# Kernel optimization log

Hardware: AMD Instinct MI355X
Metric: run time of the kernel (lower is better)

Reference implementation:

```python
import jax, jax.numpy as jnp
import numpy as np

HEADS = 8

def _conv1d(x, w, b, pad, groups):
    # x: (B, C_in, T), w: (C_out, C_in/groups, K)
    out = jax.lax.conv_general_dilated(
        x, w, window_strides=(1,), padding=[(pad, pad)],
        feature_group_count=groups,
        dimension_numbers=('NCH', 'OIH', 'NCH'))
    if b is not None:
        out = out + b[None, :, None]
    return out


def setup_inputs() -> dict:
    key = jax.random.key(0)
    ks = jax.random.split(key, 9)
    B, T, D, H = 8, 4096, 512, HEADS
    s = 0.02
    return {
        'x': jax.random.normal(ks[0], (B, T, D), jnp.float32),
        'W_qkv': jax.random.normal(ks[1], (D, 3 * D), jnp.float32) * s,
        'w_qkv_dw': jax.random.normal(ks[2], (3 * D, 1, 3), jnp.float32) * s,
        'w_ctx1': jax.random.normal(ks[3], (D, 1, 3), jnp.float32) * s,
        'w_ctx2': jax.random.normal(ks[4], (D, 1, 5), jnp.float32) * s,
        'W_fc': jax.random.normal(ks[5], (3 * H, 9), jnp.float32) * s,
        'b_fc': jnp.zeros((9,), jnp.float32),
        'w_dep': jax.random.normal(ks[6], (D, 9, 3), jnp.float32) * s,
        'b_dep': jnp.zeros((D,), jnp.float32),
        'temperature': jnp.ones((H, 1, 1), jnp.float32),
    }


def reference(x, W_qkv, w_qkv_dw, w_ctx1, w_ctx2, W_fc, b_fc, w_dep, b_dep, temperature):
    B, T, D = x.shape
    H = HEADS
    C = D // H  # channels per head

    # qkv linear + depthwise conv (k=3)
    qkv = x @ W_qkv                                       # (B,T,3D)
    qkv = _conv1d(qkv.transpose(0, 2, 1), w_qkv_dw, None, 1, 3 * D).transpose(0, 2, 1)

    # fc branch: (B,T,3H,C) -> fc over the 3H axis -> (B,T,9,C)
    f_all = qkv.reshape(B, T, 3 * H, C)
    f = jnp.einsum('bthc,hn->btnc', f_all, W_fc) + b_fc[None, None, :, None]
    f_conv = f.reshape(B, T, 9 * C).transpose(0, 2, 1)    # (B, 9C, T)
    out_conv = _conv1d(f_conv, w_dep, b_dep, 1, C).transpose(0, 2, 1)  # (B,T,D)

    # channel attention: q,k,v -> (B,H,C,T), L2-normalize over T
    q, k, v = jnp.split(qkv, 3, axis=-1)
    def to_heads(z):
        return z.reshape(B, T, H, C).transpose(0, 2, 3, 1)  # (B,H,C,T)
    q, k, v = to_heads(q), to_heads(k), to_heads(v)
    q = q / jnp.maximum(jnp.linalg.norm(q, axis=-1, keepdims=True), 1e-12)
    k = k / jnp.maximum(jnp.linalg.norm(k, axis=-1, keepdims=True), 1e-12)
    attn = jnp.einsum('bhct,bhdt->bhcd', q, k) * temperature  # (B,H,C,C)
    attn = jax.nn.softmax(attn, axis=-1)
    out_att = jnp.einsum('bhcd,bhdt->bhct', attn, v)
    out_att = out_att.transpose(0, 3, 1, 2).reshape(B, T, D)

    # regional context: depthwise k=3 -> ReLU -> depthwise k=5
    ctx = _conv1d(x.transpose(0, 2, 1), w_ctx1, None, 1, D)
    ctx = jax.nn.relu(ctx)
    ctx = _conv1d(ctx, w_ctx2, None, 2, D).transpose(0, 2, 1)

    return ctx + out_conv + out_att
```

## Files before the change

kernel.cpp:

```cpp
#include <hip/hip_runtime.h>

typedef __attribute__((ext_vector_type(8))) _Float16 f16x8;
typedef __attribute__((ext_vector_type(4))) _Float16 f16x4;
typedef __attribute__((ext_vector_type(4))) float f32x4;

__device__ inline void gl_lds16(const void* g, void* l) {
  __builtin_amdgcn_global_load_lds(
      (const __attribute__((address_space(1))) unsigned int*)g,
      (__attribute__((address_space(3))) unsigned int*)l, 16, 0, 0);
}

__global__ __launch_bounds__(256) void zero_k(float* __restrict__ g, float* __restrict__ n) {
  int i = (blockIdx.x << 8) + threadIdx.x;
  if (i < 262144) g[i] = 0.f;
  if (i < 12288) n[i] = 0.f;
}

__global__ __launch_bounds__(256) void split_x_k(
    const float* __restrict__ x, _Float16* __restrict__ hi) {
  int i = (blockIdx.x << 8) + threadIdx.x;
  float4 v = ((const float4*)x)[i];
  f16x4 h;
  h[0] = (_Float16)v.x; h[1] = (_Float16)v.y;
  h[2] = (_Float16)v.z; h[3] = (_Float16)v.w;
  *(f16x4*)&hi[(size_t)i << 2] = h;
}

__global__ __launch_bounds__(256) void split_wt_k(
    const float* __restrict__ w, _Float16* __restrict__ hi) {
  __shared__ float tile[32][33];
  int k0 = blockIdx.x << 5;
  int n0 = blockIdx.y << 5;
  int r = threadIdx.x >> 5, c = threadIdx.x & 31;
#pragma unroll
  for (int i = 0; i < 4; ++i)
    tile[r + (i << 3)][c] = w[(size_t)(k0 + r + (i << 3)) * 1536 + n0 + c];
  __syncthreads();
#pragma unroll
  for (int i = 0; i < 4; ++i) {
    int n = r + (i << 3), k = c;
    hi[(size_t)(n0 + n) * 512 + k0 + k] = (_Float16)tile[k][n];
  }
}

__global__ __launch_bounds__(256) void gemm_qkv_k(
    const _Float16* __restrict__ xhi, const _Float16* __restrict__ whi,
    _Float16* __restrict__ qkv) {
  __shared__ _Float16 As[3][128 * 32];
  __shared__ _Float16 Bs[3][128 * 32];
  const int tid = threadIdx.x;
  const int wave = tid >> 6, lane = tid & 63;
  const int orig = blockIdx.x;
  const int wg = ((orig & 7) * 384) + (orig >> 3);
  const int bm = wg / 12;
  const int bn = wg - bm * 12;
  const int wm = (wave >> 1) << 6, wn = (wave & 1) << 6;
  const int lhi = lane >> 4, llo = lane & 15;

  f32x4 zero = {};
  f32x4 acc[4][4];
#pragma unroll
  for (int i = 0; i < 4; ++i)
#pragma unroll
    for (int j = 0; j < 4; ++j) acc[i][j] = zero;

  const int srowA = (bm << 7) + (wave << 5) + (lane >> 2);
  const int srowB = (bn << 7) + (wave << 5) + (lane >> 2);
  const int kc = (((lane & 3) ^ ((lane >> 3) & 3)) << 3);
  const size_t aoff0 = ((size_t)srowA << 9) + kc;
  const size_t aoff1 = ((size_t)(srowA + 16) << 9) + kc;
  const size_t boff0 = ((size_t)srowB << 9) + kc;
  const size_t boff1 = ((size_t)(srowB + 16) << 9) + kc;
  const int wb0 = (wave << 5) << 5;
  const int wb1 = ((wave << 5) + 16) << 5;

  auto stage = [&](int buf, int kk) {
    const int k0 = kk << 5;
    gl_lds16(xhi + aoff0 + k0, &As[buf][wb0]);
    gl_lds16(xhi + aoff1 + k0, &As[buf][wb1]);
    gl_lds16(whi + boff0 + k0, &Bs[buf][wb0]);
    gl_lds16(whi + boff1 + k0, &Bs[buf][wb1]);
  };

  stage(0, 0);
  stage(1, 1);
  int cur = 0;
  for (int kk = 0; kk < 16; ++kk) {
    if (kk < 14) {
      stage((cur + 2) % 3, kk + 2);
      asm volatile("s_waitcnt vmcnt(8)" ::: "memory");
    } else if (kk == 14) {
      asm volatile("s_waitcnt vmcnt(4)" ::: "memory");
    } else {
      asm volatile("s_waitcnt vmcnt(0)" ::: "memory");
    }
    __builtin_amdgcn_s_barrier();
    __builtin_amdgcn_sched_barrier(0);
    const int ksw = ((lhi ^ ((llo >> 1) & 3)) << 3);
    f16x8 af[4], bf[4];
#pragma unroll
    for (int mi = 0; mi < 4; ++mi)
      af[mi] = *(const f16x8*)&As[cur][((wm + (mi << 4) + llo) << 5) + ksw];
#pragma unroll
    for (int ni = 0; ni < 4; ++ni)
      bf[ni] = *(const f16x8*)&Bs[cur][((wn + (ni << 4) + llo) << 5) + ksw];
    __builtin_amdgcn_s_setprio(1);
#pragma unroll
    for (int mi = 0; mi < 4; ++mi)
#pragma unroll
      for (int ni = 0; ni < 4; ++ni)
        acc[mi][ni] = __builtin_amdgcn_mfma_f32_16x16x32_f16(af[mi], bf[ni], acc[mi][ni], 0, 0, 0);
    __builtin_amdgcn_s_setprio(0);
    __builtin_amdgcn_sched_barrier(0);
    __builtin_amdgcn_s_barrier();
    cur = (cur + 1) % 3;
  }
#pragma unroll
  for (int mi = 0; mi < 4; ++mi) {
    const int row0 = (bm << 7) + wm + (mi << 4) + (lhi << 2);
#pragma unroll
    for (int ni = 0; ni < 4; ++ni) {
      const int col = (bn << 7) + wn + (ni << 4) + llo;
      _Float16* p = qkv + (size_t)row0 * 1536 + col;
#pragma unroll
      for (int r = 0; r < 4; ++r) p[(size_t)r * 1536] = (_Float16)acc[mi][ni][r];
    }
  }
}

__global__ __launch_bounds__(384) void dwconv_k(
    const _Float16* __restrict__ qkv, const float* __restrict__ w3,
    _Float16* __restrict__ qkvc, float* __restrict__ partials) {
  __shared__ float ssb[192][8];
  const int tid = threadIdx.x;
  const int sub = (tid >= 192) ? 1 : 0;
  const int g = tid - sub * 192;
  const int c0 = g << 3;
  const int blk = blockIdx.x;
  const int b = blk >> 6;
  const int pair = blk & 63;
  const int t0 = (pair << 6) + (sub << 5);
  const _Float16* base = qkv + ((size_t)((b << 12) + t0)) * 1536 + c0;
  _Float16* obase = qkvc + ((size_t)((b << 12) + t0)) * 1536 + c0;
  float w0[8], w1[8], w2[8];
#pragma unroll
  for (int j = 0; j < 8; ++j) {
    w0[j] = w3[(c0 + j) * 3 + 0];
    w1[j] = w3[(c0 + j) * 3 + 1];
    w2[j] = w3[(c0 + j) * 3 + 2];
  }
  f16x8 zero8 = {};
  f16x8 pv = (t0 == 0) ? zero8 : *(const f16x8*)&base[-1536];
  f16x8 cv = *(const f16x8*)&base[0];
  float ss[8] = {};
#pragma unroll 4
  for (int i = 0; i < 32; ++i) {
    f16x8 nv = (t0 + i == 4095) ? zero8 : *(const f16x8*)&base[(size_t)(i + 1) * 1536];
    f16x8 o;
#pragma unroll
    for (int j = 0; j < 8; ++j) {
      float of = (float)pv[j] * w0[j] + (float)cv[j] * w1[j] + (float)nv[j] * w2[j];
      _Float16 oh = (_Float16)of;
      o[j] = oh;
      float orf = (float)oh;
      ss[j] += orf * orf;
    }
    *(f16x8*)&obase[(size_t)i * 1536] = o;
    pv = cv; cv = nv;
  }
  if (sub) {
#pragma unroll
    for (int j = 0; j < 8; ++j) ssb[g][j] = ss[j];
  }
  __syncthreads();
  if (!sub) {
    float* pp = partials + ((size_t)pair) * 12288 + b * 1536 + c0;
    *(float4*)pp = make_float4(ss[0] + ssb[g][0], ss[1] + ssb[g][1],
                               ss[2] + ssb[g][2], ss[3] + ssb[g][3]);
    *(float4*)(pp + 4) = make_float4(ss[4] + ssb[g][4], ss[5] + ssb[g][5],
                                     ss[6] + ssb[g][6], ss[7] + ssb[g][7]);
  }
}

__global__ __launch_bounds__(256) void reduce_norms_k(
    const float* __restrict__ partials, float* __restrict__ norms) {
  int i = (blockIdx.x << 8) + threadIdx.x;
  float s = 0.f;
  for (int ch = 0; ch < 64; ++ch) s += partials[(size_t)ch * 12288 + i];
  norms[i] = s;
}

__global__ __launch_bounds__(256) void attn_gram_k(
    const _Float16* __restrict__ qkvc, float* __restrict__ Gbuf) {
  int bh = blockIdx.x;  int b = bh >> 3, h = bh & 7;
  int tq = blockIdx.y;
  __shared__ _Float16 qT[64][136];
  __shared__ _Float16 kT[64][136];
  const int tid = threadIdx.x;
  const int wave = tid >> 6, lane = tid & 63;
  const int lhi = lane >> 4, llo = lane & 15;
  const int coff = h << 6;
  const int c0 = wave << 4;

  f32x4 zero = {};
  f32x4 acc[4];
#pragma unroll
  for (int i = 0; i < 4; ++i) acc[i] = zero;

  for (int ch = 0; ch < 2; ++ch) {
    __syncthreads();
#pragma unroll
    for (int i = 0; i < 4; ++i) {
      int idx = (i << 8) + tid;
      int tl = idx >> 3, g = idx & 7;
      int t = (tq << 8) + (ch << 7) + tl;
      const _Float16* gp = qkvc + ((size_t)((b << 12) + t)) * 1536 + coff + (g << 3);
      f16x8 qv = *(const f16x8*)gp;
      f16x8 kv = *(const f16x8*)(gp + 512);
#pragma unroll
      for (int j = 0; j < 8; ++j) {
        qT[(g << 3) + j][tl] = qv[j];
        kT[(g << 3) + j][tl] = kv[j];
      }
    }
    __syncthreads();
#pragma unroll
    for (int kt = 0; kt < 4; ++kt) {
      const int toff = (kt << 5) + (lhi << 3);
      f16x8 af = *(const f16x8*)&qT[c0 + llo][toff];
#pragma unroll
      for (int di = 0; di < 4; ++di) {
        f16x8 bf = *(const f16x8*)&kT[(di << 4) + llo][toff];
        acc[di] = __builtin_amdgcn_mfma_f32_16x16x32_f16(af, bf, acc[di], 0, 0, 0);
      }
    }
  }
  float* Gp = Gbuf + ((size_t)bh << 12);
#pragma unroll
  for (int di = 0; di < 4; ++di)
#pragma unroll
    for (int r = 0; r < 4; ++r)
      atomicAdd(&Gp[(c0 + (lhi << 2) + r) * 64 + (di << 4) + llo], acc[di][r]);
}

__global__ __launch_bounds__(256) void attn_softmax_k(
    const float* __restrict__ Gbuf, const float* __restrict__ norms,
    const float* __restrict__ temp, float* __restrict__ attn) {
  int tid = threadIdx.x;
  int sub = tid >> 6, c = tid & 63;
  int bh = (blockIdx.x << 2) + sub;
  int b = bh >> 3, h = bh & 7;
  __shared__ float nk[4][64];
  float nq = fmaxf(sqrtf(norms[b * 1536 + (h << 6) + c]), 1e-12f);
  nk[sub][c] = fmaxf(sqrtf(norms[b * 1536 + 512 + (h << 6) + c]), 1e-12f);
  __syncthreads();
  float inq = temp[h] / nq;
  const float* Gp = Gbuf + ((size_t)bh << 12) + c * 64;
  float mx = -3.0e38f;
  for (int d = 0; d < 64; ++d) mx = fmaxf(mx, Gp[d] / nk[sub][d] * inq);
  float s = 0.f;
  for (int d = 0; d < 64; ++d) s += expf(Gp[d] / nk[sub][d] * inq - mx);
  float inv = 1.0f / s;
  float* op = attn + ((size_t)bh << 12) + c * 64;
  for (int d = 0; d < 64; ++d) op[d] = expf(Gp[d] / nk[sub][d] * inq - mx) * inv;
}

__global__ __launch_bounds__(256) void attn_out_k(
    const _Float16* __restrict__ qkvc, const float* __restrict__ attn,
    float* __restrict__ out) {
  int blk = blockIdx.x;
  int tt = blk & 31, h = (blk >> 5) & 7, b = blk >> 8;
  int t0 = tt << 7;
  __shared__ float atT[64][68];
  __shared__ float vbT[64][132];
  int tid = threadIdx.x;
  const float* ap = attn + ((size_t)((b << 3) + h) << 12);
#pragma unroll
  for (int i = 0; i < 16; ++i) {
    int idx = (i << 8) + tid;  int c2 = idx >> 6, e = idx & 63;
    atT[e][c2] = ap[idx];
  }
#pragma unroll
  for (int i = 0; i < 4; ++i) {
    int idx = (i << 8) + tid;
    int t = idx >> 3, e8 = (idx & 7) << 3;
    f16x8 v = *(const f16x8*)&qkvc[((size_t)((b << 12) + t0 + t)) * 1536 + 1024 + (h << 6) + e8];
#pragma unroll
    for (int j = 0; j < 8; ++j) vbT[e8 + j][t] = (float)v[j];
  }
  __syncthreads();
  int tg = tid >> 4, cg = tid & 15;
  float acc[8][4] = {};
#pragma unroll 2
  for (int e = 0; e < 64; ++e) {
    float4 av = *(const float4*)&atT[e][cg << 2];
    float4 v0 = *(const float4*)&vbT[e][tg << 3];
    float4 v1 = *(const float4*)&vbT[e][(tg << 3) + 4];
    float va[8] = {v0.x, v0.y, v0.z, v0.w, v1.x, v1.y, v1.z, v1.w};
    float aa[4] = {av.x, av.y, av.z, av.w};
#pragma unroll
    for (int j = 0; j < 8; ++j)
#pragma unroll
      for (int i = 0; i < 4; ++i) acc[j][i] += va[j] * aa[i];
  }
#pragma unroll
  for (int j = 0; j < 8; ++j) {
    int t = t0 + (tg << 3) + j;
    float* op = &out[(((size_t)((b << 12) + t)) << 9) + (h << 6) + (cg << 2)];
    float4 prev = *(const float4*)op;
    float4 st = make_float4(acc[j][0] + prev.x, acc[j][1] + prev.y,
                            acc[j][2] + prev.z, acc[j][3] + prev.w);
    *(float4*)op = st;
  }
}

__global__ __launch_bounds__(256) void conv2_k(
    const _Float16* __restrict__ qkvc, const float* __restrict__ x,
    const float* __restrict__ wfc, const float* __restrict__ bfc,
    const float* __restrict__ wdep, const float* __restrict__ bdep,
    const float* __restrict__ w1, const float* __restrict__ w2,
    float* __restrict__ out) {
  __shared__ _Float16 fs[18][576];
  __shared__ float wfcs[216];
  __shared__ float bfcs[9];
  int b = blockIdx.x >> 8;
  int t0 = (blockIdx.x & 255) << 4;
  int tid = threadIdx.x;
  if (tid < 216) wfcs[tid] = wfc[tid];
  else if (tid < 225) bfcs[tid - 216] = bfc[tid - 216];
  __syncthreads();

  if (tid < 144) {
    int row = tid / 8, cg = tid & 7;
    int t = t0 - 1 + row;
    int cbase = cg << 3;
    if (t >= 0 && t < 4096) {
      const _Float16* q = qkvc + ((size_t)((b << 12) + t)) * 1536 + cbase;
      float acc9[9][8];
#pragma unroll
      for (int n = 0; n < 9; ++n) {
        float bv = bfcs[n];
#pragma unroll
        for (int j = 0; j < 8; ++j) acc9[n][j] = bv;
      }
      for (int m = 0; m < 24; ++m) {
        f16x8 v = *(const f16x8*)&q[m << 6];
        float vf[8];
#pragma unroll
        for (int j = 0; j < 8; ++j) vf[j] = (float)v[j];
#pragma unroll
        for (int n = 0; n < 9; ++n) {
          float w = wfcs[m * 9 + n];
#pragma unroll
          for (int j = 0; j < 8; ++j) acc9[n][j] += w * vf[j];
        }
      }
#pragma unroll
      for (int n = 0; n < 9; ++n) {
        f16x8 o;
#pragma unroll
        for (int j = 0; j < 8; ++j) o[j] = (_Float16)acc9[n][j];
        *(f16x8*)&fs[row][(n << 6) + cbase] = o;
      }
    } else {
      f16x8 z = {};
#pragma unroll
      for (int n = 0; n < 9; ++n) *(f16x8*)&fs[row][(n << 6) + cbase] = z;
    }
  }
  __syncthreads();

#pragma unroll
  for (int pass = 0; pass < 2; ++pass) {
    int o = (pass << 8) + tid;
    int g9 = (o >> 3) * 9;
    float wd[27];
#pragma unroll
    for (int q = 0; q < 27; ++q) wd[q] = wdep[o * 27 + q];
    float w2r[5];
#pragma unroll
    for (int p = 0; p < 5; ++p) w2r[p] = w2[o * 5 + p];
    float bd = bdep[o];
    float w10 = w1[o * 3], w11 = w1[o * 3 + 1], w12 = w1[o * 3 + 2];
    const float* xb = x + ((size_t)(b << 12)) * 512 + o;

    int tp0 = t0 - 2;
    float xm = (tp0 - 1 >= 0) ? xb[(size_t)(tp0 - 1) * 512] : 0.f;
    float xc = (tp0 >= 0 && tp0 < 4096) ? xb[(size_t)tp0 * 512] : 0.f;
    float cv4[4];
#pragma unroll
    for (int i = 0; i < 4; ++i) {
      int tp = tp0 + i;
      float xp = (tp + 1 >= 0 && tp + 1 < 4096) ? xb[(size_t)(tp + 1) * 512] : 0.f;
      float v = 0.f;
      if (tp >= 0 && tp < 4096)
        v = fmaxf(xm * w10 + xc * w11 + xp * w12, 0.f);
      cv4[i] = (float)(_Float16)v;
      xm = xc; xc = xp;
    }
    float c0 = cv4[0], cA = cv4[1], cB = cv4[2], cC = cv4[3];

    float f0[9], f1[9], f2[9];
#pragma unroll
    for (int i = 0; i < 9; ++i) {
      f0[i] = (float)fs[0][g9 + i];
      f1[i] = (float)fs[1][g9 + i];
    }
    float* ob = out + ((size_t)((b << 12) + t0)) * 512 + o;
    for (int tl = 0; tl < 16; ++tl) {
      int tp = t0 + 2 + tl;
      float xp = (tp + 1 < 4096) ? xb[(size_t)(tp + 1) * 512] : 0.f;
      float v4 = 0.f;
      if (tp < 4096) v4 = fmaxf(xm * w10 + xc * w11 + xp * w12, 0.f);
      float c4 = (float)(_Float16)v4;
      xm = xc; xc = xp;

      float s = bd;
#pragma unroll
      for (int i = 0; i < 9; ++i) f2[i] = (float)fs[tl + 2][g9 + i];
#pragma unroll
      for (int i = 0; i < 9; ++i)
        s += f0[i] * wd[i * 3 + 0] + f1[i] * wd[i * 3 + 1] + f2[i] * wd[i * 3 + 2];
      s += c0 * w2r[0] + cA * w2r[1] + cB * w2r[2] + cC * w2r[3] + c4 * w2r[4];
      ob[(size_t)tl * 512] = s;
#pragma unroll
      for (int i = 0; i < 9; ++i) { f0[i] = f1[i]; f1[i] = f2[i]; }
      c0 = cA; cA = cB; cB = cC; cC = c4;
    }
  }
}

extern "C" void kernel_launch(void* const* d_in, const int* in_sizes, int n_in,
                              void* d_out, int out_size, void* d_ws, size_t ws_size,
                              hipStream_t stream) {
  (void)in_sizes; (void)n_in; (void)out_size; (void)ws_size;
  const float* x        = (const float*)d_in[0];
  const float* W_qkv    = (const float*)d_in[1];
  const float* w_qkv_dw = (const float*)d_in[2];
  const float* w_ctx1   = (const float*)d_in[3];
  const float* w_ctx2   = (const float*)d_in[4];
  const float* W_fc     = (const float*)d_in[5];
  const float* b_fc     = (const float*)d_in[6];
  const float* w_dep    = (const float*)d_in[7];
  const float* b_dep    = (const float*)d_in[8];
  const float* temperature = (const float*)d_in[9];
  float* out = (float*)d_out;

  char* ws = (char*)d_ws;
  _Float16* xhi  = (_Float16*)(ws);
  _Float16* whi  = (_Float16*)(ws + 100663296);
  float* partials = (float*)(ws + 100663296);
  _Float16* qkv16  = (_Float16*)(ws + 103809024);
  _Float16* qkvc16 = (_Float16*)(ws);
  char* tail = ws + 204472320;
  float* Gbuf  = (float*)(tail);
  float* attn  = (float*)(tail + 1048576);
  float* norms = (float*)(tail + 2097152);

  zero_k<<<1024, 256, 0, stream>>>(Gbuf, norms);
  split_x_k<<<16384, 256, 0, stream>>>(x, xhi);
  split_wt_k<<<dim3(16, 48), 256, 0, stream>>>(W_qkv, whi);
  gemm_qkv_k<<<3072, 256, 0, stream>>>(xhi, whi, qkv16);
  dwconv_k<<<512, 384, 0, stream>>>(qkv16, w_qkv_dw, qkvc16, partials);
  reduce_norms_k<<<48, 256, 0, stream>>>(partials, norms);
  conv2_k<<<2048, 256, 0, stream>>>(qkvc16, x, W_fc, b_fc, w_dep, b_dep,
                                    w_ctx1, w_ctx2, out);
  attn_gram_k<<<dim3(64, 16), 256, 0, stream>>>(qkvc16, Gbuf);
  attn_softmax_k<<<16, 256, 0, stream>>>(Gbuf, norms, temperature, attn);
  attn_out_k<<<2048, 256, 0, stream>>>(qkvc16, attn, out);
}
```

Before: 293.5 us.

## Enlarge QKV GEMM tiles to 256x256 with 512 threads and 4-stage LDS pipeline

Each QKV GEMM workgroup now computes a 256x256 output tile with 8 waves instead of a 128x128 tile with 4 waves. Each wave owns a 128x64 sub-tile, which raises arithmetic intensity per LDS and global load. The LDS ring grows from three to four stages with a deeper vmcnt wait, and A fragments are loaded inside the MFMA loop to save registers. The trade-off is one workgroup per CU with about 128KB of LDS and a bigger accumulator footprint, which lowers occupancy and may raise register pressure.

After: 298.6 us. No clear change (+1.7%).

```diff
diff --git a/kernel.cpp b/kernel.cpp
--- a/kernel.cpp
+++ b/kernel.cpp
@@ -43,85 +43,88 @@
   }
 }
 
-__global__ __launch_bounds__(256) void gemm_qkv_k(
+__global__ __launch_bounds__(512, 1) void gemm_qkv_k(
     const _Float16* __restrict__ xhi, const _Float16* __restrict__ whi,
     _Float16* __restrict__ qkv) {
-  __shared__ _Float16 As[3][128 * 32];
-  __shared__ _Float16 Bs[3][128 * 32];
+  __shared__ _Float16 As[4][256 * 32];
+  __shared__ _Float16 Bs[4][256 * 32];
   const int tid = threadIdx.x;
-  const int wave = tid >> 6, lane = tid & 63;
+  const int lane = tid & 63;
+  const int wave = tid >> 6;
   const int orig = blockIdx.x;
-  const int wg = ((orig & 7) * 384) + (orig >> 3);
-  const int bm = wg / 12;
-  const int bn = wg - bm * 12;
-  const int wm = (wave >> 1) << 6, wn = (wave & 1) << 6;
+  const int wg = ((orig & 7) * 96) + (orig >> 3);
+  const int bm = wg / 6;
+  const int bn = wg - bm * 6;
+  const int wm = (wave >> 2) << 7;
+  const int wn = (wave & 3) << 6;
   const int lhi = lane >> 4, llo = lane & 15;
 
   f32x4 zero = {};
-  f32x4 acc[4][4];
-#pragma unroll
-  for (int i = 0; i < 4; ++i)
+  f32x4 acc[8][4];
+#pragma unroll
+  for (int i = 0; i < 8; ++i)
 #pragma unroll
     for (int j = 0; j < 4; ++j) acc[i][j] = zero;
 
-  const int srowA = (bm << 7) + (wave << 5) + (lane >> 2);
-  const int srowB = (bn << 7) + (wave << 5) + (lane >> 2);
-  const int kc = (((lane & 3) ^ ((lane >> 3) & 3)) << 3);
-  const size_t aoff0 = ((size_t)srowA << 9) + kc;
-  const size_t aoff1 = ((size_t)(srowA + 16) << 9) + kc;
-  const size_t boff0 = ((size_t)srowB << 9) + kc;
-  const size_t boff1 = ((size_t)(srowB + 16) << 9) + kc;
-  const int wb0 = (wave << 5) << 5;
-  const int wb1 = ((wave << 5) + 16) << 5;
-
-  auto stage = [&](int buf, int kk) {
-    const int k0 = kk << 5;
-    gl_lds16(xhi + aoff0 + k0, &As[buf][wb0]);
-    gl_lds16(xhi + aoff1 + k0, &As[buf][wb1]);
-    gl_lds16(whi + boff0 + k0, &Bs[buf][wb0]);
-    gl_lds16(whi + boff1 + k0, &Bs[buf][wb1]);
+  const int row0 = tid >> 2;
+  const int srcc = (((tid & 3) ^ ((tid >> 3) & 3)) << 3);
+  const size_t arow0 = (size_t)(bm * 256 + row0) * 512;
+  const size_t arow1 = (size_t)(bm * 256 + 128 + row0) * 512;
+  const size_t brow0 = (size_t)(bn * 256 + row0) * 512;
+  const size_t brow1 = (size_t)(bn * 256 + 128 + row0) * 512;
+  const int ld0 = tid << 3;
+  const int ld1 = 4096 + (tid << 3);
+
+  auto stage_pair = [&](int p) {
+    const int reg = p & 3;
+    const int kof = ((p >> 1) << 6) + ((p & 1) << 5) + srcc;
+    gl_lds16(xhi + arow0 + kof, &As[reg][ld0]);
+    gl_lds16(xhi + arow1 + kof, &As[reg][ld1]);
+    gl_lds16(whi + brow0 + kof, &Bs[reg][ld0]);
+    gl_lds16(whi + brow1 + kof, &Bs[reg][ld1]);
   };
 
-  stage(0, 0);
-  stage(1, 1);
-  int cur = 0;
-  for (int kk = 0; kk < 16; ++kk) {
-    if (kk < 14) {
-      stage((cur + 2) % 3, kk + 2);
+  stage_pair(0); stage_pair(1); stage_pair(2);
+  const int ksw = ((lhi ^ ((llo >> 1) & 3)) << 3);
+
+  for (int ph = 0; ph < 16; ++ph) {
+    if (ph <= 12) stage_pair(ph + 3);
+    if (ph <= 12) {
+      asm volatile("s_waitcnt vmcnt(12)" ::: "memory");
+    } else if (ph == 13) {
       asm volatile("s_waitcnt vmcnt(8)" ::: "memory");
-    } else if (kk == 14) {
+    } else if (ph == 14) {
       asm volatile("s_waitcnt vmcnt(4)" ::: "memory");
     } else {
       asm volatile("s_waitcnt vmcnt(0)" ::: "memory");
     }
     __builtin_amdgcn_s_barrier();
     __builtin_amdgcn_sched_barrier(0);
-    const int ksw = ((lhi ^ ((llo >> 1) & 3)) << 3);
-    f16x8 af[4], bf[4];
-#pragma unroll
-    for (int mi = 0; mi < 4; ++mi)
-      af[mi] = *(const f16x8*)&As[cur][((wm + (mi << 4) + llo) << 5) + ksw];
+    const int reg = ph & 3;
+    f16x8 bf[4];
 #pragma unroll
     for (int ni = 0; ni < 4; ++ni)
-      bf[ni] = *(const f16x8*)&Bs[cur][((wn + (ni << 4) + llo) << 5) + ksw];
+      bf[ni] = *(const f16x8*)&Bs[reg][(wn + (ni << 4) + llo) * 32 + ksw];
     __builtin_amdgcn_s_setprio(1);
 #pragma unroll
-    for (int mi = 0; mi < 4; ++mi)
-#pragma unroll
-      for (int ni = 0; ni < 4; ++ni)
-        acc[mi][ni] = __builtin_amdgcn_mfma_f32_16x16x32_f16(af[mi], bf[ni], acc[mi][ni], 0, 0, 0);
+    for (int mi = 0; mi < 8; ++mi) {
+      f16x8 af = *(const f16x8*)&As[reg][(wm + (mi << 4) + llo) * 32 + ksw];
+      acc[mi][0] = __builtin_amdgcn_mfma_f32_16x16x32_f16(af, bf[0], acc[mi][0], 0, 0, 0);
+      acc[mi][1] = __builtin_amdgcn_mfma_f32_16x16x32_f16(af, bf[1], acc[mi][1], 0, 0, 0);
+      acc[mi][2] = __builtin_amdgcn_mfma_f32_16x16x32_f16(af, bf[2], acc[mi][2], 0, 0, 0);
+      acc[mi][3] = __builtin_amdgcn_mfma_f32_16x16x32_f16(af, bf[3], acc[mi][3], 0, 0, 0);
+    }
     __builtin_amdgcn_s_setprio(0);
     __builtin_amdgcn_sched_barrier(0);
     __builtin_amdgcn_s_barrier();
-    cur = (cur + 1) % 3;
-  }
-#pragma unroll
-  for (int mi = 0; mi < 4; ++mi) {
-    const int row0 = (bm << 7) + wm + (mi << 4) + (lhi << 2);
+  }
+#pragma unroll
+  for (int mi = 0; mi < 8; ++mi) {
+    const int r0 = (bm << 8) + wm + (mi << 4) + (lhi << 2);
 #pragma unroll
     for (int ni = 0; ni < 4; ++ni) {
-      const int col = (bn << 7) + wn + (ni << 4) + llo;
-      _Float16* p = qkv + (size_t)row0 * 1536 + col;
+      const int col = (bn << 8) + wn + (ni << 4) + llo;
+      _Float16* p = qkv + (size_t)r0 * 1536 + col;
 #pragma unroll
       for (int r = 0; r < 4; ++r) p[(size_t)r * 1536] = (_Float16)acc[mi][ni][r];
     }
@@ -460,7 +463,7 @@
   zero_k<<<1024, 256, 0, stream>>>(Gbuf, norms);
   split_x_k<<<16384, 256, 0, stream>>>(x, xhi);
   split_wt_k<<<dim3(16, 48), 256, 0, stream>>>(W_qkv, whi);
-  gemm_qkv_k<<<3072, 256, 0, stream>>>(xhi, whi, qkv16);
+  gemm_qkv_k<<<768, 512, 0, stream>>>(xhi, whi, qkv16);
   dwconv_k<<<512, 384, 0, stream>>>(qkv16, w_qkv_dw, qkvc16, partials);
   reduce_norms_k<<<48, 256, 0, stream>>>(partials, norms);
   conv2_k<<<2048, 256, 0, stream>>>(qkvc16, x, W_fc, b_fc, w_dep, b_dep,
```
